# Kernel tuning notes

Measured on AMD Instinct MI355X. Metric: run time of the kernel, lower is better.

The kernel has to match this reference:

```python
import jax, jax.numpy as jnp
import numpy as np

D = 512       # input_dim
K = 8         # output_size (number of bilinear slices)
L = 64        # hash_length
Q = 4096      # number of query vectors
C = 4096      # number of class vectors


def setup_inputs() -> dict:
    key = jax.random.key(0)
    ks = jax.random.split(key, 8)
    class_vector = jax.random.normal(ks[0], (C, D), dtype=jnp.float32)
    query_vector = jax.random.normal(ks[1], (Q, D), dtype=jnp.float32)
    # xavier_normal over (D, D, K): std = sqrt(2 / (fan_in + fan_out))
    xav = float(np.sqrt(2.0 / (D + D)))
    M = jax.random.normal(ks[2], (D, D, K), dtype=jnp.float32) * xav
    # score_layer: Linear(K, 1)
    lim_s = 1.0 / np.sqrt(K)
    score_w = jax.random.uniform(ks[3], (K,), jnp.float32, -lim_s, lim_s)
    score_b = jax.random.uniform(ks[4], (1,), jnp.float32, -lim_s, lim_s)
    # hash_layer: Linear(D, L) + Tanh
    lim_h = 1.0 / np.sqrt(D)
    hash_w = jax.random.uniform(ks[5], (L, D), jnp.float32, -lim_h, lim_h)
    hash_b = jax.random.uniform(ks[6], (L,), jnp.float32, -lim_h, lim_h)
    return {
        "class_vector": class_vector,
        "query_vector": query_vector,
        "M": M,
        "score_w": score_w,
        "score_b": score_b,
        "hash_w": hash_w,
        "hash_b": hash_b,
    }


def reference(class_vector, query_vector, M, score_w, score_b, hash_w, hash_b):
    # Looped bilinear product fused into one einsum:
    # inter_k = Q @ (C @ M[:,:,k]).T  ->  [Q, C, K]
    bi = jnp.einsum('ci,ijk,qj->qck', class_vector, M, query_vector)
    act = jax.nn.relu(bi)
    # score_layer: Linear(K, 1) then squeeze -> [Q, C]
    other = jnp.einsum('qck,k->qc', act, score_w) + score_b[0]
    relation_scores = jax.nn.softmax(other, axis=1)       # softmax over class dim
    query_features = relation_scores @ class_vector + query_vector  # [Q, D]
    hash_codes = jnp.tanh(query_features @ hash_w.T + hash_b)       # [Q, L]
    return hash_codes
```

## Files before the change

kernel.cpp:

```cpp
#include <hip/hip_runtime.h>
#include <hip/hip_bf16.h>
#include <math.h>

#define D_ 512
#define K_ 8
#define L_ 64
#define Q_ 4096
#define C_ 4096
#define N_ (C_ * K_)

typedef short short8 __attribute__((ext_vector_type(8)));
typedef float f32x4 __attribute__((ext_vector_type(4)));

static __device__ __forceinline__ void split2(float v, unsigned short& h, unsigned short& l) {
    __hip_bfloat16 hh = __float2bfloat16(v);
    float r = v - __bfloat162float(hh);
    __hip_bfloat16 ll = __float2bfloat16(r);
    h = *reinterpret_cast<unsigned short*>(&hh);
    l = *reinterpret_cast<unsigned short*>(&ll);
}

#define ASYNC_COPY16(gp, lp)                                                        \
    __builtin_amdgcn_global_load_lds((const __attribute__((address_space(1))) void*)(gp), \
                                     (__attribute__((address_space(3))) void*)(lp), \
                                     16, 0, 0)

__global__ void split_f32(const float* __restrict__ x,
                          unsigned short* __restrict__ hi,
                          unsigned short* __restrict__ lo) {
    int i = blockIdx.x * blockDim.x + threadIdx.x;
    split2(x[i], hi[i], lo[i]);
}

__global__ void transpose_M_split_tiled(const float* __restrict__ M,
                                        unsigned short* __restrict__ Mh,
                                        unsigned short* __restrict__ Ml) {
    __shared__ float t[64 * 65];
    const int t0 = blockIdx.x * 64;
    const int i0 = blockIdx.y * 64;
    const int tid = threadIdx.x;
#pragma unroll
    for (int it = 0; it < 16; ++it) {
        int idx = tid + it * 256;
        int ri = idx >> 6, tc = idx & 63;
        t[tc * 65 + ri] = M[(size_t)(i0 + ri) * 4096 + t0 + tc];
    }
    __syncthreads();
    const int j0 = t0 >> 3;
#pragma unroll
    for (int it = 0; it < 16; ++it) {
        int odx = tid + it * 256;
        int tl = odx >> 6, ic = odx & 63;
        int n2 = (tl & 7) * 512 + j0 + (tl >> 3);
        size_t o = (size_t)n2 * 512 + i0 + ic;
        split2(t[tl * 65 + ic], Mh[o], Ml[o]);
    }
}

__global__ void transpose_classT_tiled(const float* __restrict__ x,
                                       unsigned short* __restrict__ Th,
                                       unsigned short* __restrict__ Tl) {
    __shared__ float t[64 * 65];
    const int c0 = blockIdx.x * 64;
    const int d0 = blockIdx.y * 64;
    const int tid = threadIdx.x;
#pragma unroll
    for (int it = 0; it < 16; ++it) {
        int idx = tid + it * 256;
        int rc = idx >> 6, dc = idx & 63;
        t[dc * 65 + rc] = x[(size_t)(c0 + rc) * 512 + d0 + dc];
    }
    __syncthreads();
#pragma unroll
    for (int it = 0; it < 16; ++it) {
        int odx = tid + it * 256;
        int dr = odx >> 6, cc = odx & 63;
        size_t o = (size_t)(d0 + dr) * 4096 + c0 + cc;
        split2(t[dr * 65 + cc], Th[o], Tl[o]);
    }
}

#define BM1 128
#define BN1 128
#define BNW1 32
#define BKK1 32

__device__ __forceinline__ void mfma_core_nt(
    const unsigned short* __restrict__ Agh, const unsigned short* __restrict__ Agl,
    const unsigned short* __restrict__ Bgh, const unsigned short* __restrict__ Bgl,
    int lda, int ldb, int kd, int m0, int n0,
    unsigned short (*Ahb)[BM1 * BKK1], unsigned short (*Alb)[BM1 * BKK1],
    f32x4 acc[8][2]) {
    const int tid = threadIdx.x;
    const int lane = tid & 63;
    const int wid = tid >> 6;
    const int fr = lane & 15;
    const int fq = lane >> 4;
    const int co = (fq ^ ((fr >> 1) & 3)) * 8;

    const unsigned short* bh0 = Bgh + (size_t)(n0 + wid * BNW1 + fr) * ldb + fq * 8;
    const unsigned short* bl0 = Bgl + (size_t)(n0 + wid * BNW1 + fr) * ldb + fq * 8;

    short8 bh[2][2], bl[2][2];

#define STAGE_A(k0_, buf_)                                                      \
    {                                                                           \
        _Pragma("unroll")                                                       \
        for (int h = 0; h < 2; ++h) {                                           \
            const int i2 = h * 256 + tid;                                       \
            const int r = i2 >> 2;                                              \
            const int cg = (i2 & 3) ^ ((r >> 1) & 3);                           \
            const int ldsoff = (h * 256 + (tid & ~63)) * 8;                     \
            const size_t go = (size_t)(m0 + r) * lda + (k0_) + cg * 8;          \
            ASYNC_COPY16(Agh + go, &Ahb[buf_][ldsoff]);                         \
            ASYNC_COPY16(Agl + go, &Alb[buf_][ldsoff]);                         \
        }                                                                       \
    }
#define LOAD_B(k0_, g_)                                                         \
    bh[g_][0] = *(const short8*)(bh0 + (k0_));                                  \
    bh[g_][1] = *(const short8*)(bh0 + 16 * (size_t)ldb + (k0_));               \
    bl[g_][0] = *(const short8*)(bl0 + (k0_));                                  \
    bl[g_][1] = *(const short8*)(bl0 + 16 * (size_t)ldb + (k0_));

    const int niter = kd / BKK1;

    STAGE_A(0, 0)
    asm volatile("" ::: "memory");
    LOAD_B(0, 0)
    asm volatile("s_waitcnt vmcnt(4)" ::: "memory");
    __builtin_amdgcn_sched_barrier(0);
    asm volatile("s_barrier" ::: "memory");

#pragma unroll
    for (int it = 0; it < niter; ++it) {
        const int cur = it & 1, nxt = cur ^ 1;
        if (it + 1 < niter) {
            STAGE_A((it + 1) * BKK1, nxt)
        }
        asm volatile("" ::: "memory");
        if (it + 1 < niter) {
            LOAD_B((it + 1) * BKK1, nxt)
        }
#pragma unroll
        for (int mi = 0; mi < 8; ++mi) {
            const short8 ah = *(const short8*)&Ahb[cur][(mi * 16 + fr) * BKK1 + co];
            const short8 al = *(const short8*)&Alb[cur][(mi * 16 + fr) * BKK1 + co];
#pragma unroll
            for (int ni = 0; ni < 2; ++ni)
                acc[mi][ni] = __builtin_amdgcn_mfma_f32_16x16x32_bf16(ah, bh[cur][ni], acc[mi][ni], 0, 0, 0);
#pragma unroll
            for (int ni = 0; ni < 2; ++ni)
                acc[mi][ni] = __builtin_amdgcn_mfma_f32_16x16x32_bf16(ah, bl[cur][ni], acc[mi][ni], 0, 0, 0);
#pragma unroll
            for (int ni = 0; ni < 2; ++ni)
                acc[mi][ni] = __builtin_amdgcn_mfma_f32_16x16x32_bf16(al, bh[cur][ni], acc[mi][ni], 0, 0, 0);
        }
        if (it + 1 < niter) {
            asm volatile("s_waitcnt vmcnt(4)" ::: "memory");
            __builtin_amdgcn_sched_barrier(0);
            asm volatile("s_barrier" ::: "memory");
        }
    }
#undef STAGE_A
#undef LOAD_B
}

__launch_bounds__(256, 4)
__global__ void bilinear_mfma(const unsigned short* __restrict__ Qh,
                              const unsigned short* __restrict__ Ql,
                              const unsigned short* __restrict__ Ph,
                              const unsigned short* __restrict__ Pl,
                              const float* __restrict__ sw,
                              const float* __restrict__ sb,
                              float* __restrict__ other) {
    __shared__ __attribute__((aligned(16))) unsigned short Ahb[2][BM1 * BKK1];
    __shared__ __attribute__((aligned(16))) unsigned short Alb[2][BM1 * BKK1];
    const int tid = threadIdx.x;
    const int lane = tid & 63;
    const int wid = tid >> 6;
    const int fr = lane & 15;
    const int fq = lane >> 4;
    f32x4 acc[8][2] = {};
    const int q0 = blockIdx.x * BM1;
    const int n0 = blockIdx.y * BN1;
    mfma_core_nt(Qh, Ql, Ph, Pl, D_, D_, D_, q0, n0, Ahb, Alb, acc);
    const float wk = sw[lane & 7];
    const float bias = sb[0];
#pragma unroll
    for (int mi = 0; mi < 8; ++mi)
#pragma unroll
        for (int ni = 0; ni < 2; ++ni)
#pragma unroll
            for (int r = 0; r < 4; ++r) {
                float v2 = wk * fmaxf(acc[mi][ni][r], 0.f);
                v2 += __shfl_xor(v2, 1);
                v2 += __shfl_xor(v2, 2);
                v2 += __shfl_xor(v2, 4);
                if ((lane & 7) == 0) {
                    int q = q0 + mi * 16 + fq * 4 + r;
                    int c = (n0 + wid * BNW1 + ni * 16 + fr) >> 3;
                    other[(size_t)q * C_ + c] = v2 + bias;
                }
            }
}

#define OPS_ 8192
#define BUFS_ (4 * OPS_)

__device__ __forceinline__ void mfma_core8(
    const unsigned short* __restrict__ Agh, const unsigned short* __restrict__ Agl,
    const unsigned short* __restrict__ Bgh, const unsigned short* __restrict__ Bgl,
    const int lda, const int ldb, const int kd, const int m0, const int n0,
    unsigned short* Lds, f32x4 acc[8][4]) {
    const int tid = threadIdx.x;
    const int lane = tid & 63;
    const int wid = tid >> 6;
    const int fr = lane & 15;
    const int co = ((lane >> 4) ^ ((fr >> 1) & 3)) * 8;
    const int wm = (wid >> 2) * 128;
    const int wn = (wid & 3) * 64;
    const int nt = kd >> 5;
    const int aoff = (wm + fr) * 32 + co;
    const int boff = (wn + fr) * 32 + co;

#define STAGE8(k0_, buf_)                                                              \
    {                                                                                  \
        _Pragma("unroll")                                                              \
        for (int h_ = 0; h_ < 2; ++h_) {                                               \
            const int i2_ = h_ * 512 + tid;                                            \
            const int r_ = i2_ >> 2;                                                   \
            const int cg_ = (i2_ & 3) ^ ((r_ >> 1) & 3);                               \
            unsigned short* lp_ = Lds + (buf_) * BUFS_ + (h_ * 512 + (tid & ~63)) * 8; \
            const size_t ga_ = (size_t)(m0 + r_) * lda + (k0_) + cg_ * 8;              \
            const size_t gb_ = (size_t)(n0 + r_) * ldb + (k0_) + cg_ * 8;              \
            ASYNC_COPY16(Agh + ga_, lp_);                                              \
            ASYNC_COPY16(Agl + ga_, lp_ + OPS_);                                       \
            ASYNC_COPY16(Bgh + gb_, lp_ + 2 * OPS_);                                   \
            ASYNC_COPY16(Bgl + gb_, lp_ + 3 * OPS_);                                   \
        }                                                                              \
    }

#define QUAD(MH, NH)                                                                         \
    _Pragma("unroll")                                                                        \
    for (int i_ = 0; i_ < 4; ++i_) {                                                         \
        _Pragma("unroll")                                                                    \
        for (int j_ = 0; j_ < 2; ++j_) {                                                     \
            f32x4& a_ = acc[(MH) * 4 + i_][(NH) * 2 + j_];                                   \
            a_ = __builtin_amdgcn_mfma_f32_16x16x32_bf16(ah[i_], bhv[(NH) * 2 + j_], a_, 0, 0, 0); \
        }                                                                                    \
    }                                                                                        \
    _Pragma("unroll")                                                                        \
    for (int i_ = 0; i_ < 4; ++i_) {                                                         \
        _Pragma("unroll")                                                                    \
        for (int j_ = 0; j_ < 2; ++j_) {                                                     \
            f32x4& a_ = acc[(MH) * 4 + i_][(NH) * 2 + j_];                                   \
            a_ = __builtin_amdgcn_mfma_f32_16x16x32_bf16(ah[i_], blv[(NH) * 2 + j_], a_, 0, 0, 0); \
        }                                                                                    \
    }                                                                                        \
    _Pragma("unroll")                                                                        \
    for (int i_ = 0; i_ < 4; ++i_) {                                                         \
        _Pragma("unroll")                                                                    \
        for (int j_ = 0; j_ < 2; ++j_) {                                                     \
            f32x4& a_ = acc[(MH) * 4 + i_][(NH) * 2 + j_];                                   \
            a_ = __builtin_amdgcn_mfma_f32_16x16x32_bf16(al[i_], bhv[(NH) * 2 + j_], a_, 0, 0, 0); \
        }                                                                                    \
    }

    STAGE8(0, 0)
    STAGE8(32, 1)
    asm volatile("s_waitcnt vmcnt(8)" ::: "memory");
    __builtin_amdgcn_sched_barrier(0);
    __builtin_amdgcn_s_barrier();

#pragma unroll 2
    for (int t = 0; t < nt; ++t) {
        const int cur = t & 1;
        const unsigned short* Lc = Lds + cur * BUFS_;
        short8 ah[4], al[4], bhv[4], blv[4];

#pragma unroll
        for (int i = 0; i < 4; ++i) {
            ah[i] = *(const short8*)(Lc + aoff + i * 512);
            al[i] = *(const short8*)(Lc + OPS_ + aoff + i * 512);
        }
#pragma unroll
        for (int j = 0; j < 2; ++j) {
            bhv[j] = *(const short8*)(Lc + 2 * OPS_ + boff + j * 512);
            blv[j] = *(const short8*)(Lc + 3 * OPS_ + boff + j * 512);
        }
        __builtin_amdgcn_s_barrier();
        asm volatile("s_waitcnt lgkmcnt(0)" ::: "memory");
        __builtin_amdgcn_sched_barrier(0);
        __builtin_amdgcn_s_setprio(1);
        QUAD(0, 0)
        __builtin_amdgcn_s_setprio(0);
        __builtin_amdgcn_s_barrier();

#pragma unroll
        for (int j = 2; j < 4; ++j) {
            bhv[j] = *(const short8*)(Lc + 2 * OPS_ + boff + j * 512);
            blv[j] = *(const short8*)(Lc + 3 * OPS_ + boff + j * 512);
        }
        __builtin_amdgcn_s_barrier();
        asm volatile("s_waitcnt lgkmcnt(0)" ::: "memory");
        __builtin_amdgcn_sched_barrier(0);
        __builtin_amdgcn_s_setprio(1);
        QUAD(0, 1)
        __builtin_amdgcn_s_setprio(0);
        __builtin_amdgcn_s_barrier();

#pragma unroll
        for (int i = 0; i < 4; ++i) {
            ah[i] = *(const short8*)(Lc + aoff + 2048 + i * 512);
            al[i] = *(const short8*)(Lc + OPS_ + aoff + 2048 + i * 512);
        }
        __builtin_amdgcn_s_barrier();
        asm volatile("s_waitcnt lgkmcnt(0)" ::: "memory");
        __builtin_amdgcn_sched_barrier(0);
        __builtin_amdgcn_s_setprio(1);
        QUAD(1, 1)
        __builtin_amdgcn_s_setprio(0);
        __builtin_amdgcn_s_barrier();

        if (t + 2 < nt) STAGE8((t + 2) * 32, cur)
        __builtin_amdgcn_s_barrier();
        __builtin_amdgcn_s_setprio(1);
        QUAD(1, 0)
        __builtin_amdgcn_s_setprio(0);
        if (t + 2 < nt) {
            asm volatile("s_waitcnt vmcnt(8)" ::: "memory");
        } else if (t + 1 < nt) {
            asm volatile("s_waitcnt vmcnt(0)" ::: "memory");
        }
        __builtin_amdgcn_sched_barrier(0);
        __builtin_amdgcn_s_barrier();
    }
#undef STAGE8
#undef QUAD
}

__launch_bounds__(512, 2)
__global__ void gemm_P_mfma8(const unsigned short* __restrict__ Chh,
                             const unsigned short* __restrict__ Cll,
                             const unsigned short* __restrict__ Mh,
                             const unsigned short* __restrict__ Ml,
                             unsigned short* __restrict__ Ph,
                             unsigned short* __restrict__ Pl) {
    __shared__ __attribute__((aligned(16))) unsigned short Lds[2 * BUFS_];
    f32x4 acc[8][4] = {};
    const int n0 = blockIdx.x * 256;
    const int c0 = blockIdx.y * 256;
    mfma_core8(Chh, Cll, Mh, Ml, D_, D_, D_, c0, n0, Lds, acc);
    const int lane = threadIdx.x & 63;
    const int wid = threadIdx.x >> 6;
    const int fr = lane & 15, fq = lane >> 4;
    const int wm = (wid >> 2) * 128, wn = (wid & 3) * 64;
#pragma unroll
    for (int mi = 0; mi < 8; ++mi)
#pragma unroll
        for (int ni = 0; ni < 4; ++ni)
#pragma unroll
            for (int r = 0; r < 4; ++r) {
                int c = c0 + wm + mi * 16 + fq * 4 + r;
                int n2 = n0 + wn + ni * 16 + fr;
                size_t o = (size_t)c * (K_ * D_) + n2;
                split2(acc[mi][ni][r], Ph[o], Pl[o]);
            }
}

__launch_bounds__(512, 2)
__global__ void gemm_qf_mfma8(const unsigned short* __restrict__ Sh,
                              const unsigned short* __restrict__ Sl,
                              const unsigned short* __restrict__ Th,
                              const unsigned short* __restrict__ Tl,
                              float* __restrict__ qfp_base) {
    __shared__ __attribute__((aligned(16))) unsigned short Lds[2 * BUFS_];
    f32x4 acc[8][4] = {};
    const int n0 = blockIdx.x * 256;
    const int q0 = blockIdx.y * 256;
    const int zoff = blockIdx.z * (C_ / 8);
    float* qfp = qfp_base + (size_t)blockIdx.z * Q_ * D_;
    mfma_core8(Sh + zoff, Sl + zoff, Th + zoff, Tl + zoff,
               C_, C_, C_ / 8, q0, n0, Lds, acc);
    const int lane = threadIdx.x & 63;
    const int wid = threadIdx.x >> 6;
    const int fr = lane & 15, fq = lane >> 4;
    const int wm = (wid >> 2) * 128, wn = (wid & 3) * 64;
#pragma unroll
    for (int mi = 0; mi < 8; ++mi)
#pragma unroll
        for (int ni = 0; ni < 4; ++ni)
#pragma unroll
            for (int r = 0; r < 4; ++r) {
                int q = q0 + wm + mi * 16 + fq * 4 + r;
                int d = n0 + wn + ni * 16 + fr;
                qfp[(size_t)q * D_ + d] = acc[mi][ni][r];
            }
}

__launch_bounds__(256)
__global__ void softmax_split(const float* __restrict__ other,
                              unsigned short* __restrict__ Sh,
                              unsigned short* __restrict__ Sl) {
    const int q = blockIdx.x;
    const float* row = other + (size_t)q * C_;
    const int tid = threadIdx.x;
    __shared__ float red[4];
    float v[16];
    float m = -1e30f;
#pragma unroll
    for (int it = 0; it < 16; ++it) {
        v[it] = row[tid + it * 256];
        m = fmaxf(m, v[it]);
    }
#pragma unroll
    for (int off = 32; off; off >>= 1) m = fmaxf(m, __shfl_down(m, off));
    if ((tid & 63) == 0) red[tid >> 6] = m;
    __syncthreads();
    m = fmaxf(fmaxf(red[0], red[1]), fmaxf(red[2], red[3]));
    __syncthreads();
    float s = 0.f;
#pragma unroll
    for (int it = 0; it < 16; ++it) {
        v[it] = __expf(v[it] - m);
        s += v[it];
    }
#pragma unroll
    for (int off = 32; off; off >>= 1) s += __shfl_down(s, off);
    if ((tid & 63) == 0) red[tid >> 6] = s;
    __syncthreads();
    const float inv = 1.f / (red[0] + red[1] + red[2] + red[3]);
#pragma unroll
    for (int it = 0; it < 16; ++it) {
        size_t o = (size_t)q * C_ + tid + it * 256;
        split2(v[it] * inv, Sh[o], Sl[o]);
    }
}

__launch_bounds__(256)
__global__ void hash_kernel(const float* __restrict__ qfp_base,
                            const float* __restrict__ Qv,
                            const float* __restrict__ hw,
                            const float* __restrict__ hb,
                            float* __restrict__ out) {
    __shared__ float sqf[4 * D_];
    const int q0 = blockIdx.x * 4;
    const int tid = threadIdx.x;
    {
        const float4* sq = (const float4*)&Qv[(size_t)q0 * D_];
        float4* dst = (float4*)sqf;
#pragma unroll
        for (int it = 0; it < 2; ++it) {
            int i = tid + it * 256;
            float4 o = sq[i];
#pragma unroll
            for (int z = 0; z < 8; ++z) {
                const float4 a =
                    ((const float4*)&qfp_base[(size_t)z * Q_ * D_ + (size_t)q0 * D_])[i];
                o.x += a.x; o.y += a.y; o.z += a.z; o.w += a.w;
            }
            dst[i] = o;
        }
    }
    __syncthreads();
    const int l = tid % L_;
    const int qi = tid / L_;
    float s = hb[l];
    const float* wrow = &hw[(size_t)l * D_];
    const float* xrow = &sqf[qi * D_];
#pragma unroll 4
    for (int d = 0; d < D_; d += 4) {
        float4 w4 = *(const float4*)&wrow[d];
        float4 x4 = *(const float4*)&xrow[d];
        s += x4.x * w4.x + x4.y * w4.y + x4.z * w4.z + x4.w * w4.w;
    }
    out[(size_t)(q0 + qi) * L_ + l] = tanhf(s);
}

extern "C" void kernel_launch(void* const* d_in, const int* in_sizes, int n_in,
                              void* d_out, int out_size, void* d_ws, size_t ws_size,
                              hipStream_t stream) {
    const float* class_v = (const float*)d_in[0];
    const float* query_v = (const float*)d_in[1];
    const float* M       = (const float*)d_in[2];
    const float* score_w = (const float*)d_in[3];
    const float* score_b = (const float*)d_in[4];
    const float* hash_w  = (const float*)d_in[5];
    const float* hash_b  = (const float*)d_in[6];
    float* out = (float*)d_out;

    char* base = (char*)d_ws;
    unsigned short* Ph = (unsigned short*)base;
    unsigned short* Pl = (unsigned short*)(base + (size_t)33554432);
    char* oreg          = base + (size_t)67108864;
    float* other        = (float*)oreg;
    unsigned short* Mh  = (unsigned short*)oreg;
    unsigned short* Ml  = (unsigned short*)(oreg + (size_t)4194304);
    unsigned short* Chh = (unsigned short*)(oreg + (size_t)8388608);
    unsigned short* Cll = (unsigned short*)(oreg + (size_t)12582912);
    float* qfp          = (float*)oreg;
    char* scratch = base + (size_t)134217728;
    unsigned short* Qh = (unsigned short*)scratch;
    unsigned short* Ql = (unsigned short*)(scratch + (size_t)4194304);
    unsigned short* Th = (unsigned short*)scratch;
    unsigned short* Tl = (unsigned short*)(scratch + (size_t)4194304);
    unsigned short* Sh = Ph;
    unsigned short* Sl = Pl;

    transpose_M_split_tiled<<<dim3(64, 8), 256, 0, stream>>>(M, Mh, Ml);
    split_f32<<<(C_ * D_) / 256, 256, 0, stream>>>(class_v, Chh, Cll);
    split_f32<<<(Q_ * D_) / 256, 256, 0, stream>>>(query_v, Qh, Ql);
    gemm_P_mfma8<<<dim3((K_ * D_) / 256, C_ / 256), 512, 0, stream>>>(Chh, Cll, Mh, Ml, Ph, Pl);
    bilinear_mfma<<<dim3(Q_ / BM1, N_ / BN1), 256, 0, stream>>>(Qh, Ql, Ph, Pl,
                                                                score_w, score_b, other);
    softmax_split<<<Q_, 256, 0, stream>>>(other, Sh, Sl);
    transpose_classT_tiled<<<dim3(64, 8), 256, 0, stream>>>(class_v, Th, Tl);
    gemm_qf_mfma8<<<dim3(D_ / 256, Q_ / 256, 8), 512, 0, stream>>>(Sh, Sl, Th, Tl, qfp);
    hash_kernel<<<Q_ / 4, 256, 0, stream>>>(qfp, query_v, hash_w, hash_b, out);
}
```

Baseline: 670.3 us.

## Fuse prep and softmax/transpose kernels, issue B-operand loads via inline asm

The M transpose-split and the two class/query split kernels are merged into one launch with block-range dispatch. The class/query split now uses float4 loads and ushort4 stores. The softmax kernel and the class-vector transpose-split are merged into one launch. In the bilinear MFMA core, the B-operand global loads are issued as inline-asm global_load_dwordx4 with an explicit vmcnt wait before compute, so the load-to-use ordering is controlled by hand. This cuts launch overhead and may improve load/MFMA overlap. In exchange, correctness now depends on hand-counted vmcnt values that the compiler cannot check.

New measurement: 658.8 us. No clear change (-1.7%).

```diff
diff --git a/kernel.cpp b/kernel.cpp
--- a/kernel.cpp
+++ b/kernel.cpp
@@ -25,58 +25,54 @@
                                      (__attribute__((address_space(3))) void*)(lp), \
                                      16, 0, 0)
 
-__global__ void split_f32(const float* __restrict__ x,
-                          unsigned short* __restrict__ hi,
-                          unsigned short* __restrict__ lo) {
-    int i = blockIdx.x * blockDim.x + threadIdx.x;
-    split2(x[i], hi[i], lo[i]);
-}
-
-__global__ void transpose_M_split_tiled(const float* __restrict__ M,
-                                        unsigned short* __restrict__ Mh,
-                                        unsigned short* __restrict__ Ml) {
+__global__ void fused_prep(const float* __restrict__ M,
+                           const float* __restrict__ class_v,
+                           const float* __restrict__ query_v,
+                           unsigned short* __restrict__ Mh, unsigned short* __restrict__ Ml,
+                           unsigned short* __restrict__ Chh, unsigned short* __restrict__ Cll,
+                           unsigned short* __restrict__ Qh, unsigned short* __restrict__ Ql) {
     __shared__ float t[64 * 65];
-    const int t0 = blockIdx.x * 64;
-    const int i0 = blockIdx.y * 64;
+    const int b = blockIdx.x;
     const int tid = threadIdx.x;
-#pragma unroll
-    for (int it = 0; it < 16; ++it) {
-        int idx = tid + it * 256;
-        int ri = idx >> 6, tc = idx & 63;
-        t[tc * 65 + ri] = M[(size_t)(i0 + ri) * 4096 + t0 + tc];
-    }
-    __syncthreads();
-    const int j0 = t0 >> 3;
-#pragma unroll
-    for (int it = 0; it < 16; ++it) {
-        int odx = tid + it * 256;
-        int tl = odx >> 6, ic = odx & 63;
-        int n2 = (tl & 7) * 512 + j0 + (tl >> 3);
-        size_t o = (size_t)n2 * 512 + i0 + ic;
-        split2(t[tl * 65 + ic], Mh[o], Ml[o]);
-    }
-}
-
-__global__ void transpose_classT_tiled(const float* __restrict__ x,
-                                       unsigned short* __restrict__ Th,
-                                       unsigned short* __restrict__ Tl) {
-    __shared__ float t[64 * 65];
-    const int c0 = blockIdx.x * 64;
-    const int d0 = blockIdx.y * 64;
-    const int tid = threadIdx.x;
-#pragma unroll
-    for (int it = 0; it < 16; ++it) {
-        int idx = tid + it * 256;
-        int rc = idx >> 6, dc = idx & 63;
-        t[dc * 65 + rc] = x[(size_t)(c0 + rc) * 512 + d0 + dc];
-    }
-    __syncthreads();
-#pragma unroll
-    for (int it = 0; it < 16; ++it) {
-        int odx = tid + it * 256;
-        int dr = odx >> 6, cc = odx & 63;
-        size_t o = (size_t)(d0 + dr) * 4096 + c0 + cc;
-        split2(t[dr * 65 + cc], Th[o], Tl[o]);
+    if (b < 512) {
+        const int t0 = (b & 63) * 64;
+        const int i0 = (b >> 6) * 64;
+#pragma unroll
+        for (int it = 0; it < 16; ++it) {
+            int idx = tid + it * 256;
+            int ri = idx >> 6, tc = idx & 63;
+            t[tc * 65 + ri] = M[(size_t)(i0 + ri) * 4096 + t0 + tc];
+        }
+        __syncthreads();
+        const int j0 = t0 >> 3;
+#pragma unroll
+        for (int it = 0; it < 16; ++it) {
+            int odx = tid + it * 256;
+            int tl = odx >> 6, ic = odx & 63;
+            int n2 = (tl & 7) * 512 + j0 + (tl >> 3);
+            size_t o = (size_t)n2 * 512 + i0 + ic;
+            split2(t[tl * 65 + ic], Mh[o], Ml[o]);
+        }
+    } else if (b < 2560) {
+        int i4 = ((b - 512) * 256 + tid) * 4;
+        float4 v = *(const float4*)&class_v[i4];
+        ushort4 h, l;
+        split2(v.x, h.x, l.x);
+        split2(v.y, h.y, l.y);
+        split2(v.z, h.z, l.z);
+        split2(v.w, h.w, l.w);
+        *(ushort4*)&Chh[i4] = h;
+        *(ushort4*)&Cll[i4] = l;
+    } else {
+        int i4 = ((b - 2560) * 256 + tid) * 4;
+        float4 v = *(const float4*)&query_v[i4];
+        ushort4 h, l;
+        split2(v.x, h.x, l.x);
+        split2(v.y, h.y, l.y);
+        split2(v.z, h.z, l.z);
+        split2(v.w, h.w, l.w);
+        *(ushort4*)&Qh[i4] = h;
+        *(ushort4*)&Ql[i4] = l;
     }
 }
 
@@ -98,8 +94,10 @@
     const int fq = lane >> 4;
     const int co = (fq ^ ((fr >> 1) & 3)) * 8;
 
-    const unsigned short* bh0 = Bgh + (size_t)(n0 + wid * BNW1 + fr) * ldb + fq * 8;
-    const unsigned short* bl0 = Bgl + (size_t)(n0 + wid * BNW1 + fr) * ldb + fq * 8;
+    const unsigned short* ph0 = Bgh + (size_t)(n0 + wid * BNW1 + fr) * ldb + fq * 8;
+    const unsigned short* ph1 = ph0 + 16 * (size_t)ldb;
+    const unsigned short* pl0 = Bgl + (size_t)(n0 + wid * BNW1 + fr) * ldb + fq * 8;
+    const unsigned short* pl1 = pl0 + 16 * (size_t)ldb;
 
     short8 bh[2][2], bl[2][2];
 
@@ -116,17 +114,17 @@
             ASYNC_COPY16(Agl + go, &Alb[buf_][ldsoff]);                         \
         }                                                                       \
     }
-#define LOAD_B(k0_, g_)                                                         \
-    bh[g_][0] = *(const short8*)(bh0 + (k0_));                                  \
-    bh[g_][1] = *(const short8*)(bh0 + 16 * (size_t)ldb + (k0_));               \
-    bl[g_][0] = *(const short8*)(bl0 + (k0_));                                  \
-    bl[g_][1] = *(const short8*)(bl0 + 16 * (size_t)ldb + (k0_));
+#define LOAD_B_ASM(k0_, g_)                                                               \
+    asm volatile("global_load_dwordx4 %0, %1, off" : "=v"(bh[g_][0]) : "v"(ph0 + (k0_))); \
+    asm volatile("global_load_dwordx4 %0, %1, off" : "=v"(bh[g_][1]) : "v"(ph1 + (k0_))); \
+    asm volatile("global_load_dwordx4 %0, %1, off" : "=v"(bl[g_][0]) : "v"(pl0 + (k0_))); \
+    asm volatile("global_load_dwordx4 %0, %1, off" : "=v"(bl[g_][1]) : "v"(pl1 + (k0_)));
 
     const int niter = kd / BKK1;
 
     STAGE_A(0, 0)
     asm volatile("" ::: "memory");
-    LOAD_B(0, 0)
+    LOAD_B_ASM(0, 0)
     asm volatile("s_waitcnt vmcnt(4)" ::: "memory");
     __builtin_amdgcn_sched_barrier(0);
     asm volatile("s_barrier" ::: "memory");
@@ -139,8 +137,14 @@
         }
         asm volatile("" ::: "memory");
         if (it + 1 < niter) {
-            LOAD_B((it + 1) * BKK1, nxt)
-        }
+            LOAD_B_ASM((it + 1) * BKK1, nxt)
+        }
+        if (it + 1 < niter) {
+            asm volatile("s_waitcnt vmcnt(8)" ::: "memory");
+        } else {
+            asm volatile("s_waitcnt vmcnt(0)" ::: "memory");
+        }
+        __builtin_amdgcn_sched_barrier(0);
 #pragma unroll
         for (int mi = 0; mi < 8; ++mi) {
             const short8 ah = *(const short8*)&Ahb[cur][(mi * 16 + fr) * BKK1 + co];
@@ -162,7 +166,7 @@
         }
     }
 #undef STAGE_A
-#undef LOAD_B
+#undef LOAD_B_ASM
 }
 
 __launch_bounds__(256, 4)
@@ -399,41 +403,65 @@
 }
 
 __launch_bounds__(256)
-__global__ void softmax_split(const float* __restrict__ other,
-                              unsigned short* __restrict__ Sh,
-                              unsigned short* __restrict__ Sl) {
-    const int q = blockIdx.x;
-    const float* row = other + (size_t)q * C_;
+__global__ void fused_softmax_tc(const float* __restrict__ other,
+                                 unsigned short* __restrict__ Sh,
+                                 unsigned short* __restrict__ Sl,
+                                 const float* __restrict__ class_v,
+                                 unsigned short* __restrict__ Th,
+                                 unsigned short* __restrict__ Tl) {
+    __shared__ float smem[64 * 65];
+    const int b = blockIdx.x;
     const int tid = threadIdx.x;
-    __shared__ float red[4];
-    float v[16];
-    float m = -1e30f;
-#pragma unroll
-    for (int it = 0; it < 16; ++it) {
-        v[it] = row[tid + it * 256];
-        m = fmaxf(m, v[it]);
-    }
-#pragma unroll
-    for (int off = 32; off; off >>= 1) m = fmaxf(m, __shfl_down(m, off));
-    if ((tid & 63) == 0) red[tid >> 6] = m;
-    __syncthreads();
-    m = fmaxf(fmaxf(red[0], red[1]), fmaxf(red[2], red[3]));
-    __syncthreads();
-    float s = 0.f;
-#pragma unroll
-    for (int it = 0; it < 16; ++it) {
-        v[it] = __expf(v[it] - m);
-        s += v[it];
-    }
-#pragma unroll
-    for (int off = 32; off; off >>= 1) s += __shfl_down(s, off);
-    if ((tid & 63) == 0) red[tid >> 6] = s;
-    __syncthreads();
-    const float inv = 1.f / (red[0] + red[1] + red[2] + red[3]);
-#pragma unroll
-    for (int it = 0; it < 16; ++it) {
-        size_t o = (size_t)q * C_ + tid + it * 256;
-        split2(v[it] * inv, Sh[o], Sl[o]);
+    if (b < 4096) {
+        const int q = b;
+        const float* row = other + (size_t)q * C_;
+        float v[16];
+        float m = -1e30f;
+#pragma unroll
+        for (int it = 0; it < 16; ++it) {
+            v[it] = row[tid + it * 256];
+            m = fmaxf(m, v[it]);
+        }
+#pragma unroll
+        for (int off = 32; off; off >>= 1) m = fmaxf(m, __shfl_down(m, off));
+        if ((tid & 63) == 0) smem[tid >> 6] = m;
+        __syncthreads();
+        m = fmaxf(fmaxf(smem[0], smem[1]), fmaxf(smem[2], smem[3]));
+        __syncthreads();
+        float s = 0.f;
+#pragma unroll
+        for (int it = 0; it < 16; ++it) {
+            v[it] = __expf(v[it] - m);
+            s += v[it];
+        }
+#pragma unroll
+        for (int off = 32; off; off >>= 1) s += __shfl_down(s, off);
+        if ((tid & 63) == 0) smem[tid >> 6] = s;
+        __syncthreads();
+        const float inv = 1.f / (smem[0] + smem[1] + smem[2] + smem[3]);
+#pragma unroll
+        for (int it = 0; it < 16; ++it) {
+            size_t o = (size_t)q * C_ + tid + it * 256;
+            split2(v[it] * inv, Sh[o], Sl[o]);
+        }
+    } else {
+        const int bb = b - 4096;
+        const int c0 = (bb & 63) * 64;
+        const int d0 = (bb >> 6) * 64;
+#pragma unroll
+        for (int it = 0; it < 16; ++it) {
+            int idx = tid + it * 256;
+            int rc = idx >> 6, dc = idx & 63;
+            smem[dc * 65 + rc] = class_v[(size_t)(c0 + rc) * 512 + d0 + dc];
+        }
+        __syncthreads();
+#pragma unroll
+        for (int it = 0; it < 16; ++it) {
+            int odx = tid + it * 256;
+            int dr = odx >> 6, cc = odx & 63;
+            size_t o = (size_t)(d0 + dr) * 4096 + c0 + cc;
+            split2(smem[dr * 65 + cc], Th[o], Tl[o]);
+        }
     }
 }
 
@@ -507,14 +535,11 @@
     unsigned short* Sh = Ph;
     unsigned short* Sl = Pl;
 
-    transpose_M_split_tiled<<<dim3(64, 8), 256, 0, stream>>>(M, Mh, Ml);
-    split_f32<<<(C_ * D_) / 256, 256, 0, stream>>>(class_v, Chh, Cll);
-    split_f32<<<(Q_ * D_) / 256, 256, 0, stream>>>(query_v, Qh, Ql);
+    fused_prep<<<4608, 256, 0, stream>>>(M, class_v, query_v, Mh, Ml, Chh, Cll, Qh, Ql);
     gemm_P_mfma8<<<dim3((K_ * D_) / 256, C_ / 256), 512, 0, stream>>>(Chh, Cll, Mh, Ml, Ph, Pl);
     bilinear_mfma<<<dim3(Q_ / BM1, N_ / BN1), 256, 0, stream>>>(Qh, Ql, Ph, Pl,
                                                                 score_w, score_b, other);
-    softmax_split<<<Q_, 256, 0, stream>>>(other, Sh, Sl);
-    transpose_classT_tiled<<<dim3(64, 8), 256, 0, stream>>>(class_v, Th, Tl);
+    fused_softmax_tc<<<4608, 256, 0, stream>>>(other, Sh, Sl, class_v, Th, Tl);
     gemm_qf_mfma8<<<dim3(D_ / 256, Q_ / 256, 8), 512, 0, stream>>>(Sh, Sl, Th, Tl, qfp);
     hash_kernel<<<Q_ / 4, 256, 0, stream>>>(qfp, query_v, hash_w, hash_b, out);
 }
```
